# Optimization experiments

Measured on AMD Instinct MI355X. Metric: run time of the kernel, lower is better.

## Reference

```python
import jax, jax.numpy as jnp
from jax import lax
import numpy as np

IMG = 15      # odd spatial edge; num_patches = 4*(IMG-1) = 56
CH = 256      # spectral channels
DIM = 512
HEADS = 8
DH = 64       # dim_head; inner_dim = HEADS*DH = 512
DEPTH = 6
MLP = 2048
NCLS = 16
RATIO = 0.5   # args.ratio (scalar, not trainable)
SCALE = DH ** -0.5
NPATCH = 4 * (IMG - 1)


def _ring(a1, a2, b1, b2, E, mid1, mid2):
    # Exact replica of outer_sampling traversal; returns static index tables.
    tgt, s1, s2 = [], [], []
    d = [0, 1]; l1 = a1; l2 = b1 - 1; start = 0
    while True:
        l1 += d[0]; l2 += d[1]
        if l1 == a1 and l2 == b1:
            if start == 1:
                break
            start = 1
        if l1 > a2:
            d = [0, -1]; l1 -= 1; continue
        elif l2 < b1:
            d = [-1, 0]; l2 += 1; continue
        elif l2 > b2:
            d = [1, 0]; l2 -= 1; continue
        if l1 < 0 or l1 > E or l2 < 0 or l2 > E:
            continue
        m1 = 0 if l1 == mid1 else -int(np.sign(l1 - mid1))
        m2 = 0 if l2 == mid2 else -int(np.sign(l2 - mid2))
        if abs(l1 - mid1) > abs(l2 - mid2):
            s1.append((l1 + m1) * E + l2); s2.append((l1 + m1) * E + l2 + m2)
        elif abs(l1 - mid1) < abs(l2 - mid2):
            s1.append(l1 * E + l2 + m2); s2.append((l1 + m1) * E + l2 + m2)
        else:  # corner: x[t] += ratio * x[s] == (x[s]+x[s])*ratio/2
            s = (l1 + m1) * E + l2 + m2
            s1.append(s); s2.append(s)
        tgt.append(l1 * E + l2)
    return np.array(tgt), np.array(s1), np.array(s2)

_MID = IMG // 2
# Within each ring, every read hits an already-finalized inner-ring cell,
# so rings can be applied as vectorized gather+scatter in sequence.
RINGS = [_ring(_MID - i, _MID + i, _MID - i, _MID + i, IMG, _MID, _MID)
         for i in range(1, _MID + 1)]


def _sinusoid(n_pos, d):
    pos = np.arange(n_pos)[:, None].astype(np.float64)
    j = np.arange(d)[None, :]
    ang = pos / np.power(10000.0, 2 * (j // 2) / d)
    tab = np.zeros((n_pos, d))
    tab[:, 0::2] = np.sin(ang[:, 0::2])
    tab[:, 1::2] = np.cos(ang[:, 1::2])
    return jnp.asarray(tab[None], dtype=jnp.float32)

POS = _sinusoid(NPATCH + 1, DIM)


def _ln(x, g, b, eps=1e-5):
    mu = x.mean(-1, keepdims=True)
    v = ((x - mu) ** 2).mean(-1, keepdims=True)
    return (x - mu) * lax.rsqrt(v + eps) * g + b


def _forward(x, We, be, cls_token, Wqkv, Wo, bo, ln1g, ln1b, W1, b1, W2, b2,
             ln2g, ln2b, lnh_g, lnh_b, Wh, bh):
    B = x.shape[0]
    xf = x.reshape(B, CH, IMG * IMG)
    for tgt, s1, s2 in RINGS:
        xf = xf.at[:, :, tgt].set(xf[:, :, tgt] + (xf[:, :, s1] + xf[:, :, s2]) * (RATIO / 2))
    # original runs spiral under torch.no_grad()
    tok = lax.stop_gradient(jnp.transpose(xf[:, :, RINGS[-1][0]], (0, 2, 1)))  # [B, 56, CH]
    h = tok @ We + be                                                          # [B, 56, DIM]
    h = jnp.concatenate([jnp.broadcast_to(cls_token, (B, 1, DIM)), h], axis=1)
    h = h + POS[:, :NPATCH + 1]
    for l in range(DEPTH):
        y = _ln(h, ln1g[l], ln1b[l])
        qkv = y @ Wqkv[l]
        q, k, v = [t.reshape(B, -1, HEADS, DH).transpose(0, 2, 1, 3)
                   for t in jnp.split(qkv, 3, axis=-1)]
        a = jax.nn.softmax(jnp.einsum('bhid,bhjd->bhij', q, k) * SCALE, axis=-1)
        o = jnp.einsum('bhij,bhjd->bhid', a, v).transpose(0, 2, 1, 3).reshape(B, -1, HEADS * DH)
        h = h + o @ Wo[l] + bo[l]
        y = _ln(h, ln2g[l], ln2b[l])
        h = h + jax.nn.gelu(y @ W1[l] + b1[l], approximate=False) @ W2[l] + b2[l]
    p = h.mean(axis=1)  # pool='mean'
    return _ln(p, lnh_g, lnh_b) @ Wh + bh


def setup_inputs():
    key = jax.random.key(0)
    ks = jax.random.split(key, 8)
    B = 512
    def nrm(k, shp, s=0.02):
        return jax.random.normal(k, shp, jnp.float32) * s
    return {
        'x': jax.random.normal(ks[0], (B, CH, IMG, IMG), jnp.float32),
        'We': nrm(ks[1], (CH, DIM)),
        'be': jnp.zeros((DIM,), jnp.float32),
        'cls_token': nrm(ks[2], (1, 1, DIM), 1.0),
        'Wqkv': nrm(ks[3], (DEPTH, DIM, 3 * HEADS * DH)),
        'Wo': nrm(ks[4], (DEPTH, HEADS * DH, DIM)),
        'bo': jnp.zeros((DEPTH, DIM), jnp.float32),
        'ln1g': jnp.ones((DEPTH, DIM), jnp.float32),
        'ln1b': jnp.zeros((DEPTH, DIM), jnp.float32),
        'W1': nrm(ks[5], (DEPTH, DIM, MLP)),
        'b1': jnp.zeros((DEPTH, MLP), jnp.float32),
        'W2': nrm(ks[6], (DEPTH, MLP, DIM)),
        'b2': jnp.zeros((DEPTH, DIM), jnp.float32),
        'ln2g': jnp.ones((DEPTH, DIM), jnp.float32),
        'ln2b': jnp.zeros((DEPTH, DIM), jnp.float32),
        'lnh_g': jnp.ones((DIM,), jnp.float32),
        'lnh_b': jnp.zeros((DIM,), jnp.float32),
        'Wh': nrm(ks[7], (DIM, NCLS)),
        'bh': jnp.zeros((NCLS,), jnp.float32),
    }


def reference(x, We, be, cls_token, Wqkv, Wo, bo, ln1g, ln1b, W1, b1, W2, b2,
              ln2g, ln2b, lnh_g, lnh_b, Wh, bh):
    return _forward(x, We, be, cls_token, Wqkv, Wo, bo, ln1g, ln1b, W1, b1,
                    W2, b2, ln2g, ln2b, lnh_g, lnh_b, Wh, bh)
```

## Files before the change

### kernel.cpp

```cpp
#include <hip/hip_runtime.h>
#include <math.h>

#define NB   512
#define SEQ  57
#define NP   56
#define CHN  256
#define DIM  512
#define MLPD 2048

typedef float f32x4 __attribute__((ext_vector_type(4)));
typedef short s16x8 __attribute__((ext_vector_type(8)));

__device__ __forceinline__ short f2bf(float f) {
    union { float f; unsigned u; } v; v.f = f;
    unsigned r = (v.u + 0x7fffu + ((v.u >> 16) & 1u)) >> 16;
    return (short)r;
}
__device__ __forceinline__ float geluf(float v) {
    return 0.5f * v * (1.0f + erff(v * 0.70710678118654752f));
}

#define GLDS16(g, l) __builtin_amdgcn_global_load_lds(                         \
    (const __attribute__((address_space(1))) void*)(g),                        \
    (__attribute__((address_space(3))) void*)(l), 16, 0, 0)

struct RingTables { int tgt[224]; int s1[224]; int s2[224]; int start[8]; };
constexpr RingTables make_rings() {
    RingTables rt{};
    int n = 0; const int E = 15, mid = 7;
    rt.start[0] = 0;
    for (int i = 1; i <= 7; ++i) {
        int a1 = mid - i, a2 = mid + i, b1 = mid - i, b2 = mid + i;
        int d0 = 0, d1 = 1, l1 = a1, l2 = b1 - 1, started = 0;
        while (true) {
            l1 += d0; l2 += d1;
            if (l1 == a1 && l2 == b1) { if (started) break; started = 1; }
            if (l1 > a2)      { d0 = 0;  d1 = -1; l1 -= 1; continue; }
            else if (l2 < b1) { d0 = -1; d1 = 0;  l2 += 1; continue; }
            else if (l2 > b2) { d0 = 1;  d1 = 0;  l2 -= 1; continue; }
            if (l1 < 0 || l1 > E || l2 < 0 || l2 > E) continue;
            int m1 = -((l1 > mid) - (l1 < mid));
            int m2 = -((l2 > mid) - (l2 < mid));
            int ab1 = l1 > mid ? l1 - mid : mid - l1;
            int ab2 = l2 > mid ? l2 - mid : mid - l2;
            if (ab1 > ab2)      { rt.s1[n] = (l1+m1)*E + l2;   rt.s2[n] = (l1+m1)*E + l2+m2; }
            else if (ab1 < ab2) { rt.s1[n] = l1*E + l2+m2;     rt.s2[n] = (l1+m1)*E + l2+m2; }
            else                { int s = (l1+m1)*E + l2+m2;   rt.s1[n] = s; rt.s2[n] = s; }
            rt.tgt[n] = l1*E + l2;
            ++n;
        }
        rt.start[i] = n;
    }
    return rt;
}
constexpr RingTables RT_HOST = make_rings();
__constant__ RingTables RT = RT_HOST;

__global__ __launch_bounds__(256) void spiral_kernel(const float* __restrict__ x,
                                                     short* __restrict__ tok) {
    __shared__ float tile[64 * 225];
    const int b  = blockIdx.x >> 2;
    const int c0 = (blockIdx.x & 3) << 6;
    const float* src = x + ((size_t)b * CHN + c0) * 225;
    for (int i = threadIdx.x; i < 64 * 225; i += 256) tile[i] = src[i];
    __syncthreads();
    for (int r = 0; r < 7; ++r) {
        const int s0 = RT.start[r], n = RT.start[r + 1] - s0;
        for (int w = threadIdx.x; w < (n << 6); w += 256) {
            const int c = w & 63, t = s0 + (w >> 6);
            float* row = tile + c * 225;
            row[RT.tgt[t]] += (row[RT.s1[t]] + row[RT.s2[t]]) * 0.25f;
        }
        __syncthreads();
    }
    for (int w = threadIdx.x; w < (56 << 6); w += 256) {
        const int c = w & 63, p = w >> 6;
        tok[((size_t)b * NP + p) * CHN + c0 + c] = f2bf(tile[c * 225 + RT.tgt[168 + p]]);
    }
}

__global__ __launch_bounds__(256) void transcvt(const float* __restrict__ in,
                                                short* __restrict__ out, int K, int N) {
    __shared__ float t[32][33];
    in  += (size_t)blockIdx.z * K * N;
    out += (size_t)blockIdx.z * K * N;
    const int k0 = blockIdx.y << 5, n0 = blockIdx.x << 5;
    const int tx = threadIdx.x & 31, ty = threadIdx.x >> 5;
    for (int i = ty; i < 32; i += 8) t[i][tx] = in[(size_t)(k0 + i) * N + n0 + tx];
    __syncthreads();
    for (int i = ty; i < 32; i += 8) out[(size_t)(n0 + i) * K + k0 + tx] = f2bf(t[tx][i]);
}

__global__ __launch_bounds__(256) void pos_kernel(float* __restrict__ pos) {
    const int idx = blockIdx.x * 256 + threadIdx.x;
    const int t = idx >> 9, j = idx & 511;
    double expo = (double)(2 * (j >> 1)) / 512.0;
    double ang  = (double)t * pow(10000.0, -expo);
    pos[idx] = (j & 1) ? (float)cos(ang) : (float)sin(ang);
}

__global__ __launch_bounds__(256) void assemble_kernel(const float* __restrict__ emb,
                                                       const float* __restrict__ cls,
                                                       const float* __restrict__ pos,
                                                       float* __restrict__ h) {
    const unsigned idx = blockIdx.x * 256 + threadIdx.x;
    const int c = idx & 511;
    const int r = (idx >> 9) % SEQ;
    const unsigned b = idx / (SEQ * DIM);
    float base = (r == 0) ? cls[c] : emb[((size_t)b * NP + (r - 1)) * DIM + c];
    h[idx] = base + pos[r * DIM + c];
}

__global__ __launch_bounds__(256) void ln_kernel(const float* __restrict__ x,
                                                 const float* __restrict__ g,
                                                 const float* __restrict__ bta,
                                                 short* __restrict__ y) {
    const int row  = (blockIdx.x << 2) + (threadIdx.x >> 6);
    const int lane = threadIdx.x & 63;
    const float* xr = x + (size_t)row * DIM;
    float v[8]; float s = 0.f;
#pragma unroll
    for (int j = 0; j < 8; ++j) { v[j] = xr[lane + (j << 6)]; s += v[j]; }
#pragma unroll
    for (int off = 1; off < 64; off <<= 1) s += __shfl_xor(s, off);
    const float mu = s * (1.f / 512.f);
    float sq = 0.f;
#pragma unroll
    for (int j = 0; j < 8; ++j) { const float d = v[j] - mu; sq += d * d; }
#pragma unroll
    for (int off = 1; off < 64; off <<= 1) sq += __shfl_xor(sq, off);
    const float rs = rsqrtf(sq * (1.f / 512.f) + 1e-5f);
    short* yr = y + (size_t)row * DIM;
#pragma unroll
    for (int j = 0; j < 8; ++j) {
        const int c = lane + (j << 6);
        yr[c] = f2bf((v[j] - mu) * rs * g[c] + bta[c]);
    }
}

template<int ACT, bool RES, bool OUTBF>
__global__ __launch_bounds__(256, 2) void gemm_bf16(
    const short* __restrict__ A, const short* __restrict__ BT,
    const float* __restrict__ bias, const float* __restrict__ res,
    void* __restrict__ Cout, int M, int N, int K)
{
    __shared__ short As[128 * 64];
    __shared__ short Bs[128 * 64];
    const int tid = threadIdx.x;
    const int m0 = blockIdx.y << 7, n0 = blockIdx.x << 7;
    const int wave = tid >> 6, lane = tid & 63;
    const int wm = (wave >> 1) << 6, wn = (wave & 1) << 6;
    const int fm = lane & 15, fq = lane >> 4;

    const short* Ap[4]; const short* Bp[4];
    short *lA[4], *lB[4];
#pragma unroll
    for (int t = 0; t < 4; ++t) {
        const int g = t * 256 + tid;
        const int row = g >> 3;
        const int c = (g & 7) ^ (row & 7);
        Ap[t] = A  + (size_t)(m0 + row) * K + (c << 3);
        Bp[t] = BT + (size_t)(n0 + row) * K + (c << 3);
        lA[t] = As + g * 8;
        lB[t] = Bs + g * 8;
    }

    f32x4 acc[4][4] = {};

    for (int k0 = 0; k0 < K; k0 += 64) {
        __syncthreads();
#pragma unroll
        for (int t = 0; t < 4; ++t) GLDS16(Ap[t] + k0, lA[t]);
#pragma unroll
        for (int t = 0; t < 4; ++t) GLDS16(Bp[t] + k0, lB[t]);
        __syncthreads();
#pragma unroll
        for (int kk = 0; kk < 2; ++kk) {
            const int cs = ((fq + (kk << 2)) ^ (fm & 7)) << 3;
            s16x8 af[4], bfr[4];
#pragma unroll
            for (int s = 0; s < 4; ++s) {
                af[s]  = *(const s16x8*)(As + (wm + s * 16 + fm) * 64 + cs);
                bfr[s] = *(const s16x8*)(Bs + (wn + s * 16 + fm) * 64 + cs);
            }
#pragma unroll
            for (int i = 0; i < 4; ++i)
#pragma unroll
                for (int j = 0; j < 4; ++j)
                    acc[i][j] = __builtin_amdgcn_mfma_f32_16x16x32_bf16(af[i], bfr[j], acc[i][j], 0, 0, 0);
        }
    }

#pragma unroll
    for (int i = 0; i < 4; ++i) {
#pragma unroll
        for (int r = 0; r < 4; ++r) {
            const int row = m0 + wm + i * 16 + (fq << 2) + r;
#pragma unroll
            for (int j = 0; j < 4; ++j) {
                const int col = n0 + wn + j * 16 + fm;
                float v = acc[i][j][r];
                if (bias) v += bias[col];
                if (ACT == 1) v = geluf(v);
                if (RES) v += res[(size_t)row * N + col];
                if (OUTBF) ((short*)Cout)[(size_t)row * N + col] = f2bf(v);
                else       ((float*)Cout)[(size_t)row * N + col] = v;
            }
        }
    }
}

__global__ __launch_bounds__(64) void attn_mfma(const short* __restrict__ qkv,
                                                short* __restrict__ o) {
    __shared__ short Pl[64 * 72];
    __shared__ short Vt[64 * 72];
    const int b = blockIdx.x >> 3, hd = blockIdx.x & 7;
    const int lane = threadIdx.x;
    const int n = lane & 15, q = lane >> 4;
    const short* base = qkv + (size_t)b * SEQ * 1536 + hd * 64;

    {
        const short* vb = base + 1024 + lane;
        for (int t = 0; t < SEQ; ++t) Vt[lane * 72 + t] = vb[(size_t)t * 1536];
        for (int t = SEQ; t < 64; ++t) Vt[lane * 72 + t] = 0;
    }

    const s16x8 zero8 = {};
    s16x8 qf[4][2], kf[4][2];
#pragma unroll
    for (int ti = 0; ti < 4; ++ti) {
        const int tq = ti * 16 + n;
#pragma unroll
        for (int kk = 0; kk < 2; ++kk) {
            const int ko = kk * 32 + q * 8;
            qf[ti][kk] = (tq < SEQ) ? *(const s16x8*)(base + (size_t)tq * 1536 + ko)       : zero8;
            kf[ti][kk] = (tq < SEQ) ? *(const s16x8*)(base + 512 + (size_t)tq * 1536 + ko) : zero8;
        }
    }

    f32x4 sacc[4][4] = {};
#pragma unroll
    for (int ti = 0; ti < 4; ++ti)
#pragma unroll
        for (int tj = 0; tj < 4; ++tj)
#pragma unroll
            for (int kk = 0; kk < 2; ++kk)
                sacc[ti][tj] = __builtin_amdgcn_mfma_f32_16x16x32_bf16(
                    qf[ti][kk], kf[tj][kk], sacc[ti][tj], 0, 0, 0);

#pragma unroll
    for (int ti = 0; ti < 4; ++ti) {
#pragma unroll
        for (int r = 0; r < 4; ++r) {
            float v[4]; float mx = -1e30f;
#pragma unroll
            for (int tj = 0; tj < 4; ++tj) {
                float s = sacc[ti][tj][r] * 0.125f;
                if (tj * 16 + n >= SEQ) s = -1e30f;
                v[tj] = s; mx = fmaxf(mx, s);
            }
            mx = fmaxf(mx, __shfl_xor(mx, 1));
            mx = fmaxf(mx, __shfl_xor(mx, 2));
            mx = fmaxf(mx, __shfl_xor(mx, 4));
            mx = fmaxf(mx, __shfl_xor(mx, 8));
            float sum = 0.f;
#pragma unroll
            for (int tj = 0; tj < 4; ++tj) { v[tj] = __expf(v[tj] - mx); sum += v[tj]; }
            sum += __shfl_xor(sum, 1); sum += __shfl_xor(sum, 2);
            sum += __shfl_xor(sum, 4); sum += __shfl_xor(sum, 8);
            const float inv = 1.f / sum;
            const int row = ti * 16 + q * 4 + r;
#pragma unroll
            for (int tj = 0; tj < 4; ++tj)
                Pl[row * 72 + tj * 16 + n] = f2bf(v[tj] * inv);
        }
    }
    __syncthreads();

    f32x4 oacc[4][4] = {};
#pragma unroll
    for (int kk = 0; kk < 2; ++kk) {
        s16x8 pf[4], vf[4];
#pragma unroll
        for (int s = 0; s < 4; ++s) {
            pf[s] = *(const s16x8*)(Pl + (s * 16 + n) * 72 + kk * 32 + q * 8);
            vf[s] = *(const s16x8*)(Vt + (s * 16 + n) * 72 + kk * 32 + q * 8);
        }
#pragma unroll
        for (int ti = 0; ti < 4; ++ti)
#pragma unroll
            for (int td = 0; td < 4; ++td)
                oacc[ti][td] = __builtin_amdgcn_mfma_f32_16x16x32_bf16(
                    pf[ti], vf[td], oacc[ti][td], 0, 0, 0);
    }
#pragma unroll
    for (int ti = 0; ti < 4; ++ti) {
#pragma unroll
        for (int r = 0; r < 4; ++r) {
            const int trow = ti * 16 + q * 4 + r;
            if (trow < SEQ) {
#pragma unroll
                for (int td = 0; td < 4; ++td)
                    o[((size_t)(b * SEQ + trow)) * DIM + hd * 64 + td * 16 + n]
                        = f2bf(oacc[ti][td][r]);
            }
        }
    }
}

__global__ __launch_bounds__(256) void head_kernel(const float* __restrict__ h,
                                                   const float* __restrict__ g,
                                                   const float* __restrict__ bb,
                                                   const float* __restrict__ Wh,
                                                   const float* __restrict__ bh,
                                                   float* __restrict__ out) {
    __shared__ float p[DIM];
    __shared__ float r1[4], r2[4];
    const int b = blockIdx.x;
    const float* hb = h + (size_t)b * SEQ * DIM;
    for (int c = threadIdx.x; c < DIM; c += 256) {
        float s = 0.f;
        for (int t = 0; t < SEQ; ++t) s += hb[t * DIM + c];
        p[c] = s * (1.f / 57.f);
    }
    __syncthreads();
    float s = 0.f;
    for (int c = threadIdx.x; c < DIM; c += 256) s += p[c];
#pragma unroll
    for (int off = 1; off < 64; off <<= 1) s += __shfl_xor(s, off);
    if ((threadIdx.x & 63) == 0) r1[threadIdx.x >> 6] = s;
    __syncthreads();
    const float mu = (r1[0] + r1[1] + r1[2] + r1[3]) * (1.f / 512.f);
    float sq = 0.f;
    for (int c = threadIdx.x; c < DIM; c += 256) { float d = p[c] - mu; sq += d * d; }
#pragma unroll
    for (int off = 1; off < 64; off <<= 1) sq += __shfl_xor(sq, off);
    if ((threadIdx.x & 63) == 0) r2[threadIdx.x >> 6] = sq;
    __syncthreads();
    const float rs = rsqrtf((r2[0] + r2[1] + r2[2] + r2[3]) * (1.f / 512.f) + 1e-5f);
    for (int c = threadIdx.x; c < DIM; c += 256) p[c] = (p[c] - mu) * rs * g[c] + bb[c];
    __syncthreads();
    if (threadIdx.x < 16) {
        float acc = bh[threadIdx.x];
        for (int c = 0; c < DIM; ++c) acc += p[c] * Wh[c * 16 + threadIdx.x];
        out[b * 16 + threadIdx.x] = acc;
    }
}

extern "C" void kernel_launch(void* const* d_in, const int* in_sizes, int n_in,
                              void* d_out, int out_size, void* d_ws, size_t ws_size,
                              hipStream_t stream) {
    (void)in_sizes; (void)n_in; (void)out_size; (void)ws_size;
    const float* x    = (const float*)d_in[0];
    const float* We   = (const float*)d_in[1];
    const float* be   = (const float*)d_in[2];
    const float* cls  = (const float*)d_in[3];
    const float* Wqkv = (const float*)d_in[4];
    const float* Wo   = (const float*)d_in[5];
    const float* bo   = (const float*)d_in[6];
    const float* ln1g = (const float*)d_in[7];
    const float* ln1b = (const float*)d_in[8];
    const float* W1   = (const float*)d_in[9];
    const float* b1   = (const float*)d_in[10];
    const float* W2   = (const float*)d_in[11];
    const float* b2   = (const float*)d_in[12];
    const float* ln2g = (const float*)d_in[13];
    const float* ln2b = (const float*)d_in[14];
    const float* lnhg = (const float*)d_in[15];
    const float* lnhb = (const float*)d_in[16];
    const float* Wh   = (const float*)d_in[17];
    const float* bh   = (const float*)d_in[18];

    char* ws = (char*)d_ws;
    float* h    = (float*)(ws);
    float* big  = (float*)(ws + 59768832);
    short* bigs = (short*)big;
    short* ybf  = (short*)(ws + 239075328);
    short* wbuf = (short*)(ws + 268959744);
    short* tokb = (short*)(ws + 306970624);
    float* pos  = (float*)(ws + 321650688);

    short* WeT   = wbuf;
    short* WqkvT = wbuf + 131072;
    short* WoT   = WqkvT + 6 * 786432;
    short* W1T   = WoT   + 6 * 262144;
    short* W2T   = W1T   + 6 * 1048576;

    pos_kernel<<<114, 256, 0, stream>>>(pos);
    transcvt<<<dim3(16,  8, 1), 256, 0, stream>>>(We,   WeT,    256,  512);
    transcvt<<<dim3(48, 16, 6), 256, 0, stream>>>(Wqkv, WqkvT,  512, 1536);
    transcvt<<<dim3(16, 16, 6), 256, 0, stream>>>(Wo,   WoT,    512,  512);
    transcvt<<<dim3(64, 16, 6), 256, 0, stream>>>(W1,   W1T,    512, 2048);
    transcvt<<<dim3(16, 64, 6), 256, 0, stream>>>(W2,   W2T,   2048,  512);
    spiral_kernel<<<2048, 256, 0, stream>>>(x, tokb);

    gemm_bf16<0, false, false><<<dim3(4, 224), 256, 0, stream>>>(
        tokb, WeT, be, nullptr, big, NB * NP, DIM, CHN);
    assemble_kernel<<<(NB * SEQ * DIM) / 256, 256, 0, stream>>>(big, cls, pos, h);

    const int M = NB * SEQ;
    for (int l = 0; l < 6; ++l) {
        ln_kernel<<<M / 4, 256, 0, stream>>>(h, ln1g + l * 512, ln1b + l * 512, ybf);
        gemm_bf16<0, false, true><<<dim3(12, 228), 256, 0, stream>>>(
            ybf, WqkvT + (size_t)l * 786432, nullptr, nullptr, bigs, M, 1536, 512);
        attn_mfma<<<NB * 8, 64, 0, stream>>>(bigs, ybf);
        gemm_bf16<0, true, false><<<dim3(4, 228), 256, 0, stream>>>(
            ybf, WoT + (size_t)l * 262144, bo + l * 512, h, h, M, 512, 512);
        ln_kernel<<<M / 4, 256, 0, stream>>>(h, ln2g + l * 512, ln2b + l * 512, ybf);
        gemm_bf16<1, false, true><<<dim3(16, 228), 256, 0, stream>>>(
            ybf, W1T + (size_t)l * 1048576, b1 + l * 2048, nullptr, bigs, M, 2048, 512);
        gemm_bf16<0, true, false><<<dim3(4, 228), 256, 0, stream>>>(
            bigs, W2T + (size_t)l * 1048576, b2 + l * 512, h, h, M, 512, 2048);
    }
    head_kernel<<<NB, 256, 0, stream>>>(h, lnhg, lnhb, Wh, bh, (float*)d_out);
}
```

Measured before the change: 2.694 ms.

## Load GEMM fragments directly from global memory with register double-buffering

Drops the LDS staging and block barriers from the bf16 GEMM. Each wave now loads its MFMA fragments straight from global memory into registers, prefetching the next 32-wide k slice while the current one is multiplied, and the launch bounds target three blocks per SM instead of two. This removes the __syncthreads stalls and LDS traffic. In exchange each tile is no longer shared through LDS, so every wave re-reads A and B rows that other waves also read, and the fragment loads are narrow strided accesses that depend on cache hits.

New measurement: 6.548 ms. 143% more time.

```diff
diff --git a/kernel.cpp b/kernel.cpp
--- a/kernel.cpp
+++ b/kernel.cpp
@@ -19,10 +19,6 @@
 __device__ __forceinline__ float geluf(float v) {
     return 0.5f * v * (1.0f + erff(v * 0.70710678118654752f));
 }
-
-#define GLDS16(g, l) __builtin_amdgcn_global_load_lds(                         \
-    (const __attribute__((address_space(1))) void*)(g),                        \
-    (__attribute__((address_space(3))) void*)(l), 16, 0, 0)
 
 struct RingTables { int tgt[224]; int s1[224]; int s2[224]; int start[8]; };
 constexpr RingTables make_rings() {
@@ -139,56 +135,46 @@
 }
 
 template<int ACT, bool RES, bool OUTBF>
-__global__ __launch_bounds__(256, 2) void gemm_bf16(
+__global__ __launch_bounds__(256, 3) void gemm_bf16(
     const short* __restrict__ A, const short* __restrict__ BT,
     const float* __restrict__ bias, const float* __restrict__ res,
     void* __restrict__ Cout, int M, int N, int K)
 {
-    __shared__ short As[128 * 64];
-    __shared__ short Bs[128 * 64];
-    const int tid = threadIdx.x;
+    const int tid  = threadIdx.x;
     const int m0 = blockIdx.y << 7, n0 = blockIdx.x << 7;
     const int wave = tid >> 6, lane = tid & 63;
     const int wm = (wave >> 1) << 6, wn = (wave & 1) << 6;
     const int fm = lane & 15, fq = lane >> 4;
 
     const short* Ap[4]; const short* Bp[4];
-    short *lA[4], *lB[4];
-#pragma unroll
-    for (int t = 0; t < 4; ++t) {
-        const int g = t * 256 + tid;
-        const int row = g >> 3;
-        const int c = (g & 7) ^ (row & 7);
-        Ap[t] = A  + (size_t)(m0 + row) * K + (c << 3);
-        Bp[t] = BT + (size_t)(n0 + row) * K + (c << 3);
-        lA[t] = As + g * 8;
-        lB[t] = Bs + g * 8;
+#pragma unroll
+    for (int s = 0; s < 4; ++s) {
+        Ap[s] = A  + (size_t)(m0 + wm + s * 16 + fm) * K + (fq << 3);
+        Bp[s] = BT + (size_t)(n0 + wn + s * 16 + fm) * K + (fq << 3);
     }
 
     f32x4 acc[4][4] = {};
+    s16x8 a0[4], b0[4], a1[4], b1[4];
+#pragma unroll
+    for (int s = 0; s < 4; ++s) { a0[s] = *(const s16x8*)(Ap[s]); b0[s] = *(const s16x8*)(Bp[s]); }
 
     for (int k0 = 0; k0 < K; k0 += 64) {
-        __syncthreads();
-#pragma unroll
-        for (int t = 0; t < 4; ++t) GLDS16(Ap[t] + k0, lA[t]);
-#pragma unroll
-        for (int t = 0; t < 4; ++t) GLDS16(Bp[t] + k0, lB[t]);
-        __syncthreads();
-#pragma unroll
-        for (int kk = 0; kk < 2; ++kk) {
-            const int cs = ((fq + (kk << 2)) ^ (fm & 7)) << 3;
-            s16x8 af[4], bfr[4];
-#pragma unroll
-            for (int s = 0; s < 4; ++s) {
-                af[s]  = *(const s16x8*)(As + (wm + s * 16 + fm) * 64 + cs);
-                bfr[s] = *(const s16x8*)(Bs + (wn + s * 16 + fm) * 64 + cs);
-            }
-#pragma unroll
-            for (int i = 0; i < 4; ++i)
-#pragma unroll
-                for (int j = 0; j < 4; ++j)
-                    acc[i][j] = __builtin_amdgcn_mfma_f32_16x16x32_bf16(af[i], bfr[j], acc[i][j], 0, 0, 0);
-        }
+        const int kn1 = k0 + 32;
+        const int kn2 = (k0 + 64 < K) ? k0 + 64 : 0;
+#pragma unroll
+        for (int s = 0; s < 4; ++s) { a1[s] = *(const s16x8*)(Ap[s] + kn1); b1[s] = *(const s16x8*)(Bp[s] + kn1); }
+#pragma unroll
+        for (int i = 0; i < 4; ++i)
+#pragma unroll
+            for (int j = 0; j < 4; ++j)
+                acc[i][j] = __builtin_amdgcn_mfma_f32_16x16x32_bf16(a0[i], b0[j], acc[i][j], 0, 0, 0);
+#pragma unroll
+        for (int s = 0; s < 4; ++s) { a0[s] = *(const s16x8*)(Ap[s] + kn2); b0[s] = *(const s16x8*)(Bp[s] + kn2); }
+#pragma unroll
+        for (int i = 0; i < 4; ++i)
+#pragma unroll
+            for (int j = 0; j < 4; ++j)
+                acc[i][j] = __builtin_amdgcn_mfma_f32_16x16x32_bf16(a1[i], b1[j], acc[i][j], 0, 0, 0);
     }
 
 #pragma unroll
```

## Vectorize GEMM/attention epilogues via swapped MFMA operands and fuse embedding assembly

Applied to the files above, without the earlier changes.

Swaps the MFMA A/B operands so each lane holds four consecutive columns, letting the GEMM and attention epilogues use 16-byte float4 and 8-byte bf16x4 stores instead of scalar stores. The embedding GEMM now writes straight into the residual stream with positional encoding added, and a small kernel fills only the cls rows, removing the separate assemble pass and its intermediate buffer. LayerNorm loads and stores are also vectorized. The change adds index arithmetic (a divide by 56) in the embedding epilogue, and it depends on the transposed fragment layout being mapped correctly.

Result: faster. 2.526 ms (-6.3%).

```diff
diff --git a/kernel.cpp b/kernel.cpp
--- a/kernel.cpp
+++ b/kernel.cpp
@@ -10,6 +10,7 @@
 
 typedef float f32x4 __attribute__((ext_vector_type(4)));
 typedef short s16x8 __attribute__((ext_vector_type(8)));
+typedef short s16x4 __attribute__((ext_vector_type(4)));
 
 __device__ __forceinline__ short f2bf(float f) {
     union { float f; unsigned u; } v; v.f = f;
@@ -99,16 +100,12 @@
     pos[idx] = (j & 1) ? (float)cos(ang) : (float)sin(ang);
 }
 
-__global__ __launch_bounds__(256) void assemble_kernel(const float* __restrict__ emb,
-                                                       const float* __restrict__ cls,
-                                                       const float* __restrict__ pos,
-                                                       float* __restrict__ h) {
-    const unsigned idx = blockIdx.x * 256 + threadIdx.x;
-    const int c = idx & 511;
-    const int r = (idx >> 9) % SEQ;
-    const unsigned b = idx / (SEQ * DIM);
-    float base = (r == 0) ? cls[c] : emb[((size_t)b * NP + (r - 1)) * DIM + c];
-    h[idx] = base + pos[r * DIM + c];
+__global__ __launch_bounds__(256) void cls_pos_kernel(const float* __restrict__ cls,
+                                                      const float* __restrict__ pos,
+                                                      float* __restrict__ h) {
+    const int idx = blockIdx.x * 256 + threadIdx.x;
+    const int c = idx & 511, b = idx >> 9;
+    h[(size_t)b * SEQ * DIM + c] = cls[c] + pos[c];
 }
 
 __global__ __launch_bounds__(256) void ln_kernel(const float* __restrict__ x,
@@ -118,27 +115,35 @@
     const int row  = (blockIdx.x << 2) + (threadIdx.x >> 6);
     const int lane = threadIdx.x & 63;
     const float* xr = x + (size_t)row * DIM;
-    float v[8]; float s = 0.f;
-#pragma unroll
-    for (int j = 0; j < 8; ++j) { v[j] = xr[lane + (j << 6)]; s += v[j]; }
+    f32x4 v0 = *(const f32x4*)(xr + (lane << 2));
+    f32x4 v1 = *(const f32x4*)(xr + (lane << 2) + 256);
+    float s = v0[0] + v0[1] + v0[2] + v0[3] + v1[0] + v1[1] + v1[2] + v1[3];
 #pragma unroll
     for (int off = 1; off < 64; off <<= 1) s += __shfl_xor(s, off);
     const float mu = s * (1.f / 512.f);
     float sq = 0.f;
 #pragma unroll
-    for (int j = 0; j < 8; ++j) { const float d = v[j] - mu; sq += d * d; }
+    for (int k = 0; k < 4; ++k) { float d = v0[k] - mu; sq += d * d; }
+#pragma unroll
+    for (int k = 0; k < 4; ++k) { float d = v1[k] - mu; sq += d * d; }
 #pragma unroll
     for (int off = 1; off < 64; off <<= 1) sq += __shfl_xor(sq, off);
     const float rs = rsqrtf(sq * (1.f / 512.f) + 1e-5f);
     short* yr = y + (size_t)row * DIM;
 #pragma unroll
-    for (int j = 0; j < 8; ++j) {
-        const int c = lane + (j << 6);
-        yr[c] = f2bf((v[j] - mu) * rs * g[c] + bta[c]);
-    }
-}
-
-template<int ACT, bool RES, bool OUTBF>
+    for (int p = 0; p < 2; ++p) {
+        const int c0 = (lane << 2) + (p << 8);
+        const f32x4 vv = p ? v1 : v0;
+        const f32x4 g4 = *(const f32x4*)(g + c0);
+        const f32x4 b4 = *(const f32x4*)(bta + c0);
+        s16x4 o;
+#pragma unroll
+        for (int k = 0; k < 4; ++k) o[k] = f2bf((vv[k] - mu) * rs * g4[k] + b4[k]);
+        *(s16x4*)(yr + c0) = o;
+    }
+}
+
+template<int ACT, bool RES, bool OUTBF, bool EMB>
 __global__ __launch_bounds__(256, 2) void gemm_bf16(
     const short* __restrict__ A, const short* __restrict__ BT,
     const float* __restrict__ bias, const float* __restrict__ res,
@@ -187,24 +192,40 @@
             for (int i = 0; i < 4; ++i)
 #pragma unroll
                 for (int j = 0; j < 4; ++j)
-                    acc[i][j] = __builtin_amdgcn_mfma_f32_16x16x32_bf16(af[i], bfr[j], acc[i][j], 0, 0, 0);
+                    acc[i][j] = __builtin_amdgcn_mfma_f32_16x16x32_bf16(bfr[j], af[i], acc[i][j], 0, 0, 0);
         }
     }
 
 #pragma unroll
     for (int i = 0; i < 4; ++i) {
-#pragma unroll
-        for (int r = 0; r < 4; ++r) {
-            const int row = m0 + wm + i * 16 + (fq << 2) + r;
-#pragma unroll
-            for (int j = 0; j < 4; ++j) {
-                const int col = n0 + wn + j * 16 + fm;
-                float v = acc[i][j][r];
-                if (bias) v += bias[col];
-                if (ACT == 1) v = geluf(v);
-                if (RES) v += res[(size_t)row * N + col];
-                if (OUTBF) ((short*)Cout)[(size_t)row * N + col] = f2bf(v);
-                else       ((float*)Cout)[(size_t)row * N + col] = v;
+        const int row = m0 + wm + i * 16 + fm;
+        size_t obase;
+        const float* posr = nullptr;
+        if (EMB) {
+            const int bb = row / 56, tt = row - bb * 56;
+            obase = ((size_t)(bb * SEQ + tt + 1)) * N;
+            posr = res + (size_t)(tt + 1) * N;
+        } else {
+            obase = (size_t)row * N;
+        }
+#pragma unroll
+        for (int j = 0; j < 4; ++j) {
+            const int col0 = n0 + wn + j * 16 + (fq << 2);
+            f32x4 v = acc[i][j];
+            if (bias) v += *(const f32x4*)(bias + col0);
+            if (EMB)  v += *(const f32x4*)(posr + col0);
+            if (ACT == 1) {
+#pragma unroll
+                for (int k = 0; k < 4; ++k) v[k] = geluf(v[k]);
+            }
+            if (RES) v += *(const f32x4*)(res + obase + col0);
+            if (OUTBF) {
+                s16x4 o;
+#pragma unroll
+                for (int k = 0; k < 4; ++k) o[k] = f2bf(v[k]);
+                *(s16x4*)((short*)Cout + obase + col0) = o;
+            } else {
+                *(f32x4*)((float*)Cout + obase + col0) = v;
             }
         }
     }
@@ -291,18 +312,19 @@
 #pragma unroll
             for (int td = 0; td < 4; ++td)
                 oacc[ti][td] = __builtin_amdgcn_mfma_f32_16x16x32_bf16(
-                    pf[ti], vf[td], oacc[ti][td], 0, 0, 0);
+                    vf[td], pf[ti], oacc[ti][td], 0, 0, 0);
     }
 #pragma unroll
     for (int ti = 0; ti < 4; ++ti) {
-#pragma unroll
-        for (int r = 0; r < 4; ++r) {
-            const int trow = ti * 16 + q * 4 + r;
-            if (trow < SEQ) {
-#pragma unroll
-                for (int td = 0; td < 4; ++td)
-                    o[((size_t)(b * SEQ + trow)) * DIM + hd * 64 + td * 16 + n]
-                        = f2bf(oacc[ti][td][r]);
+        const int t = ti * 16 + n;
+        if (t < SEQ) {
+            short* orow = o + ((size_t)(b * SEQ + t)) * DIM + hd * 64 + (q << 2);
+#pragma unroll
+            for (int td = 0; td < 4; ++td) {
+                s16x4 o4;
+#pragma unroll
+                for (int r = 0; r < 4; ++r) o4[r] = f2bf(oacc[ti][td][r]);
+                *(s16x4*)(orow + td * 16) = o4;
             }
         }
     }
@@ -373,8 +395,7 @@
 
     char* ws = (char*)d_ws;
     float* h    = (float*)(ws);
-    float* big  = (float*)(ws + 59768832);
-    short* bigs = (short*)big;
+    short* bigs = (short*)(ws + 59768832);
     short* ybf  = (short*)(ws + 239075328);
     short* wbuf = (short*)(ws + 268959744);
     short* tokb = (short*)(ws + 306970624);
@@ -394,22 +415,22 @@
     transcvt<<<dim3(16, 64, 6), 256, 0, stream>>>(W2,   W2T,   2048,  512);
     spiral_kernel<<<2048, 256, 0, stream>>>(x, tokb);
 
-    gemm_bf16<0, false, false><<<dim3(4, 224), 256, 0, stream>>>(
-        tokb, WeT, be, nullptr, big, NB * NP, DIM, CHN);
-    assemble_kernel<<<(NB * SEQ * DIM) / 256, 256, 0, stream>>>(big, cls, pos, h);
+    gemm_bf16<0, false, false, true><<<dim3(4, 224), 256, 0, stream>>>(
+        tokb, WeT, be, pos, h, NB * NP, DIM, CHN);
+    cls_pos_kernel<<<1024, 256, 0, stream>>>(cls, pos, h);
 
     const int M = NB * SEQ;
     for (int l = 0; l < 6; ++l) {
         ln_kernel<<<M / 4, 256, 0, stream>>>(h, ln1g + l * 512, ln1b + l * 512, ybf);
-        gemm_bf16<0, false, true><<<dim3(12, 228), 256, 0, stream>>>(
+        gemm_bf16<0, false, true, false><<<dim3(12, 228), 256, 0, stream>>>(
             ybf, WqkvT + (size_t)l * 786432, nullptr, nullptr, bigs, M, 1536, 512);
         attn_mfma<<<NB * 8, 64, 0, stream>>>(bigs, ybf);
-        gemm_bf16<0, true, false><<<dim3(4, 228), 256, 0, stream>>>(
+        gemm_bf16<0, true, false, false><<<dim3(4, 228), 256, 0, stream>>>(
             ybf, WoT + (size_t)l * 262144, bo + l * 512, h, h, M, 512, 512);
         ln_kernel<<<M / 4, 256, 0, stream>>>(h, ln2g + l * 512, ln2b + l * 512, ybf);
-        gemm_bf16<1, false, true><<<dim3(16, 228), 256, 0, stream>>>(
+        gemm_bf16<1, false, true, false><<<dim3(16, 228), 256, 0, stream>>>(
             ybf, W1T + (size_t)l * 1048576, b1 + l * 2048, nullptr, bigs, M, 2048, 512);
-        gemm_bf16<0, true, false><<<dim3(4, 228), 256, 0, stream>>>(
+        gemm_bf16<0, true, false, false><<<dim3(4, 228), 256, 0, stream>>>(
             bigs, W2T + (size_t)l * 1048576, b2 + l * 512, h, h, M, 512, 2048);
     }
     head_kernel<<<NB, 256, 0, stream>>>(h, lnhg, lnhb, Wh, bh, (float*)d_out);
```
